# Kernel optimization log

Measured on AMD Instinct MI355X. Metric: run time of the kernel, lower is better.

## Reference

```python
import jax, jax.numpy as jnp
import numpy as np

N = 100000      # num_node
D = 64          # latent_dim
R_EX = 8        # num_relation_ex
R_IM = 4        # num_relation_im
E_EX = 2000000  # explicit edges
E_IM = 1000000  # implicit edges


def setup_inputs() -> dict:
    key = jax.random.key(0)
    ks = jax.random.split(key, 32)
    f = lambda i, shape, s=0.05: jax.random.normal(ks[i], shape, dtype=jnp.float32) * s
    inp = {}
    inp["edge_index_ex"] = jax.random.randint(ks[0], (2, E_EX), 0, N)
    inp["edge_type_ex"] = jax.random.randint(ks[1], (E_EX,), 0, R_EX)
    inp["edge_index_im"] = jax.random.randint(ks[2], (2, E_IM), 0, N)
    inp["edge_type_im"] = jax.random.randint(ks[3], (E_IM,), 0, R_IM)
    # RGCN layer-1 (in_channels = num_node, x=None -> weight acts as per-relation embedding table)
    inp["W1_ex"] = f(4, (R_EX, N, D)); inp["root1_ex"] = f(5, (N, D)); inp["b1_ex"] = f(6, (D,))
    inp["W1_im"] = f(7, (R_IM, N, D)); inp["root1_im"] = f(8, (N, D)); inp["b1_im"] = f(9, (D,))
    # RGCN layer-2 (latent_dim -> latent_dim)
    inp["W2_ex"] = f(10, (R_EX, D, D)); inp["root2_ex"] = f(11, (D, D)); inp["b2_ex"] = f(12, (D,))
    inp["W2_im"] = f(13, (R_IM, D, D)); inp["root2_im"] = f(14, (D, D)); inp["b2_im"] = f(15, (D,))
    # ATTITU fusion head: four Linear(D, 1)
    inp["att_w11"] = f(16, (D,)); inp["att_b11"] = f(17, ())
    inp["att_w12"] = f(18, (D,)); inp["att_b12"] = f(19, ())
    inp["att_w21"] = f(20, (D,)); inp["att_b21"] = f(21, ())
    inp["att_w22"] = f(22, (D,)); inp["att_b22"] = f(23, ())
    # MLP aggregation: Linear(2D, D) -> LeakyReLU -> Linear(D, D)
    inp["agg_W1"] = f(24, (2 * D, D)); inp["agg_b1"] = f(25, (D,))
    inp["agg_W2"] = f(26, (D, D)); inp["agg_b2"] = f(27, (D,))
    return inp


def _rgcn_embed(W, root, bias, src, dst, etype, R):
    # Layer 1, x=None: out_i = root_i + bias + sum_r mean_{e: type(e)=r, dst(e)=i} W[r, src(e)]
    out = root + bias  # [N, D]
    for r in range(R):
        m = (etype == r).astype(jnp.float32)            # [E]
        msg = W[r][src] * m[:, None]                    # [E, D] relation-r embedding gather
        s = jax.ops.segment_sum(msg, dst, num_segments=N)
        c = jax.ops.segment_sum(m, dst, num_segments=N)
        out = out + s / jnp.maximum(c, 1.0)[:, None]
    return out


def _rgcn(x, W, root, bias, src, dst, etype, R):
    # Layer 2: out_i = x_i @ root + bias + sum_r (mean_{e: type=r, dst=i} x[src(e)]) @ W[r]
    out = x @ root + bias
    for r in range(R):
        m = (etype == r).astype(x.dtype)
        msg = x[src] * m[:, None]                        # [E, D]
        s = jax.ops.segment_sum(msg, dst, num_segments=N)
        c = jax.ops.segment_sum(m, dst, num_segments=N)
        h = s / jnp.maximum(c, 1.0)[:, None]             # mean-aggregated, then linear (PyG order)
        out = out + h @ W[r]
    return out


def _attitu(e1, e2, w11, b11, w12, b12, w21, b21, w22, b22):
    s1 = jax.nn.softmax(jnp.stack([e1 @ w11 + b11, e2 @ w12 + b12], axis=1), axis=1)  # [N, 2]
    f1 = s1[:, 0:1] * e1 + s1[:, 1:2] * e2
    s2 = jax.nn.softmax(jnp.stack([e1 @ w21 + b21, e2 @ w22 + b22], axis=1), axis=1)
    f2 = s2[:, 1:2] * e2 + s2[:, 0:1] * e1
    return f1, f2


def reference(edge_index_ex, edge_type_ex, edge_index_im, edge_type_im,
              W1_ex, root1_ex, b1_ex, W1_im, root1_im, b1_im,
              W2_ex, root2_ex, b2_ex, W2_im, root2_im, b2_im,
              att_w11, att_b11, att_w12, att_b12, att_w21, att_b21, att_w22, att_b22,
              agg_W1, agg_b1, agg_W2, agg_b2):
    src_ex, dst_ex = edge_index_ex[0], edge_index_ex[1]
    src_im, dst_im = edge_index_im[0], edge_index_im[1]
    ex_x1 = _rgcn_embed(W1_ex, root1_ex, b1_ex, src_ex, dst_ex, edge_type_ex, R_EX)
    im_x1 = _rgcn_embed(W1_im, root1_im, b1_im, src_im, dst_im, edge_type_im, R_IM)
    t_ex, t_im = _attitu(ex_x1, im_x1, att_w11, att_b11, att_w12, att_b12,
                         att_w21, att_b21, att_w22, att_b22)
    ex_x2 = _rgcn(t_ex, W2_ex, root2_ex, b2_ex, src_ex, dst_ex, edge_type_ex, R_EX)
    im_x2 = _rgcn(t_im, W2_im, root2_im, b2_im, src_im, dst_im, edge_type_im, R_IM)
    cat = jnp.concatenate([ex_x1 + ex_x2, im_x1 + im_x2], axis=1)  # [N, 2D]
    return jax.nn.leaky_relu(cat @ agg_W1 + agg_b1, negative_slope=0.01) @ agg_W2 + agg_b2
```

## Files before the change

### kernel.cpp

```cpp
#include <hip/hip_runtime.h>
#include <hip/hip_bf16.h>

#define N_NODE 100000
#define DIM 64
#define R_EX 8
#define R_IM 4
#define E_EX 2000000
#define E_IM 1000000
#define ND (N_NODE * DIM)

typedef __hip_bfloat16 bf16;

__device__ __forceinline__ float b2f(bf16 v) { return __bfloat162float(v); }

__device__ __forceinline__ float ldv(const void* p, long long i, int f32) {
    return f32 ? ((const float*)p)[i] : b2f(((const bf16*)p)[i]);
}

__global__ void detect_kernel(const void* probe, int* flag) {
    int t = threadIdx.x;
    float v = b2f(((const bf16*)probe)[t]);
    int bad = !(fabsf(v) <= 4.0f);
    unsigned long long m = __ballot(bad);
    if (t == 0) *flag = (m != 0ull) ? 1 : 0;
}

__global__ void count_kernel(const int* __restrict__ eidx, const int* __restrict__ etype,
                             float* __restrict__ cnt, int E) {
    int e = blockIdx.x * blockDim.x + threadIdx.x;
    if (e >= E) return;
    int dst = eidx[E + e];
    int r = etype[e];
    atomicAdd(&cnt[r * N_NODE + dst], 1.0f);
}

__global__ void inv_kernel(float* __restrict__ cnt, int n) {
    int i = blockIdx.x * blockDim.x + threadIdx.x;
    if (i >= n) return;
    cnt[i] = 1.0f / fmaxf(cnt[i], 1.0f);
}

__global__ void l1_init(const void* __restrict__ root, const void* __restrict__ bias,
                        const int* __restrict__ fp, float* __restrict__ x1) {
    int i = blockIdx.x * blockDim.x + threadIdx.x;
    if (i >= ND) return;
    int f32 = *fp;
    x1[i] = ldv(root, i, f32) + ldv(bias, i & (DIM - 1), f32);
}

__global__ void l1_edge(const int* __restrict__ eidx, const int* __restrict__ etype,
                        const void* __restrict__ W1, const float* __restrict__ inv,
                        const int* __restrict__ fp, float* __restrict__ x1, int E) {
    int gid = blockIdx.x * blockDim.x + threadIdx.x;
    int e = gid >> 6;
    int d = gid & 63;
    if (e >= E) return;
    int f32 = *fp;
    int src = eidx[e];
    int dst = eidx[E + e];
    int r = etype[e];
    float w = inv[r * N_NODE + dst];
    float v = ldv(W1, ((long long)r * N_NODE + src) * DIM + d, f32);
    atomicAdd(&x1[dst * DIM + d], v * w);
}

__global__ void attitu_kernel(const float* __restrict__ ex1, const float* __restrict__ im1,
                              const void* __restrict__ w11, const void* __restrict__ b11,
                              const void* __restrict__ w12, const void* __restrict__ b12,
                              const void* __restrict__ w21, const void* __restrict__ b21,
                              const void* __restrict__ w22, const void* __restrict__ b22,
                              const int* __restrict__ fp,
                              float* __restrict__ t_ex, float* __restrict__ t_im) {
    int gid = blockIdx.x * blockDim.x + threadIdx.x;
    int i = gid >> 6;
    int d = gid & 63;
    if (i >= N_NODE) return;
    int f32 = *fp;
    float e1 = ex1[i * DIM + d];
    float e2 = im1[i * DIM + d];
    float p11 = e1 * ldv(w11, d, f32);
    float p12 = e2 * ldv(w12, d, f32);
    float p21 = e1 * ldv(w21, d, f32);
    float p22 = e2 * ldv(w22, d, f32);
#pragma unroll
    for (int off = 32; off; off >>= 1) {
        p11 += __shfl_xor(p11, off);
        p12 += __shfl_xor(p12, off);
        p21 += __shfl_xor(p21, off);
        p22 += __shfl_xor(p22, off);
    }
    float a11 = p11 + ldv(b11, 0, f32);
    float a12 = p12 + ldv(b12, 0, f32);
    float a21 = p21 + ldv(b21, 0, f32);
    float a22 = p22 + ldv(b22, 0, f32);

    float m1 = fmaxf(a11, a12);
    float z11 = __expf(a11 - m1), z12 = __expf(a12 - m1);
    float i1 = 1.0f / (z11 + z12);
    float s10 = z11 * i1, s11 = z12 * i1;

    float m2 = fmaxf(a21, a22);
    float z21 = __expf(a21 - m2), z22 = __expf(a22 - m2);
    float i2 = 1.0f / (z21 + z22);
    float s20 = z21 * i2, s21 = z22 * i2;

    t_ex[i * DIM + d] = s10 * e1 + s11 * e2;
    t_im[i * DIM + d] = s20 * e1 + s21 * e2;
}

__global__ void l2_init_fused(const float* __restrict__ t, const void* __restrict__ root2,
                              const void* __restrict__ b2, const int* __restrict__ fp,
                              float* __restrict__ x1) {
    int gid = blockIdx.x * blockDim.x + threadIdx.x;
    int i = gid >> 6;
    int d = gid & 63;
    if (i >= N_NODE) return;
    int f32 = *fp;
    float tv = t[i * DIM + d];
    float acc = ldv(b2, d, f32) + x1[i * DIM + d];
    if (f32) {
        const float* W = (const float*)root2;
#pragma unroll
        for (int k = 0; k < DIM; ++k) acc += __shfl(tv, k) * W[k * DIM + d];
    } else {
        const bf16* W = (const bf16*)root2;
#pragma unroll
        for (int k = 0; k < DIM; ++k) acc += __shfl(tv, k) * b2f(W[k * DIM + d]);
    }
    x1[i * DIM + d] = acc;
}

__global__ void l2_agg(const int* __restrict__ eidx, const int* __restrict__ etype,
                       const float* __restrict__ t, float* __restrict__ h,
                       int E, int r0, int rc) {
    int gid = blockIdx.x * blockDim.x + threadIdx.x;
    int e = gid >> 6;
    int d = gid & 63;
    if (e >= E) return;
    int r = etype[e] - r0;
    if ((unsigned)r >= (unsigned)rc) return;
    int src = eidx[e];
    int dst = eidx[E + e];
    atomicAdd(&h[(long long)r * ND + dst * DIM + d], t[src * DIM + d]);
}

__global__ void l2_dense(const float* __restrict__ h, const void* __restrict__ W2,
                         const float* __restrict__ inv, const int* __restrict__ fp,
                         float* __restrict__ a2, int r0, int rc) {
    int gid = blockIdx.x * blockDim.x + threadIdx.x;
    int i = gid >> 6;
    int d = gid & 63;
    if (i >= N_NODE) return;
    int f32 = *fp;
    float acc = a2[i * DIM + d];
    for (int c = 0; c < rc; ++c) {
        float hv = h[(long long)c * ND + i * DIM + d];
        float w = inv[(r0 + c) * N_NODE + i];
        float s = 0.0f;
        if (f32) {
            const float* W = (const float*)W2 + (r0 + c) * DIM * DIM;
#pragma unroll
            for (int k = 0; k < DIM; ++k) s += __shfl(hv, k) * W[k * DIM + d];
        } else {
            const bf16* W = (const bf16*)W2 + (r0 + c) * DIM * DIM;
#pragma unroll
            for (int k = 0; k < DIM; ++k) s += __shfl(hv, k) * b2f(W[k * DIM + d]);
        }
        acc += w * s;
    }
    a2[i * DIM + d] = acc;
}

__global__ void l2_edge(const int* __restrict__ eidx, const int* __restrict__ etype,
                        const float* __restrict__ t, const void* __restrict__ W2,
                        const float* __restrict__ inv, const int* __restrict__ fp,
                        float* __restrict__ a2, int E) {
    int gid = blockIdx.x * blockDim.x + threadIdx.x;
    int e = gid >> 6;
    int d = gid & 63;
    if (e >= E) return;
    int f32 = *fp;
    int src = eidx[e];
    int dst = eidx[E + e];
    int r = etype[e];
    float tv = t[src * DIM + d];
    float acc = 0.0f;
    if (f32) {
        const float* W = (const float*)W2 + r * DIM * DIM;
#pragma unroll
        for (int k = 0; k < DIM; ++k) acc += __shfl(tv, k) * W[k * DIM + d];
    } else {
        const bf16* W = (const bf16*)W2 + r * DIM * DIM;
#pragma unroll
        for (int k = 0; k < DIM; ++k) acc += __shfl(tv, k) * b2f(W[k * DIM + d]);
    }
    float w = inv[r * N_NODE + dst];
    atomicAdd(&a2[dst * DIM + d], acc * w);
}

__global__ void final_kernel(const float* __restrict__ a2ex, const float* __restrict__ a2im,
                             const void* __restrict__ aggW1, const void* __restrict__ aggb1,
                             const void* __restrict__ aggW2, const void* __restrict__ aggb2,
                             const int* __restrict__ fp, void* __restrict__ out) {
    int gid = blockIdx.x * blockDim.x + threadIdx.x;
    int i = gid >> 6;
    int d = gid & 63;
    if (i >= N_NODE) return;
    int f32 = *fp;
    float cex = a2ex[i * DIM + d];
    float cim = a2im[i * DIM + d];
    float h = ldv(aggb1, d, f32);
    if (f32) {
        const float* W = (const float*)aggW1;
#pragma unroll
        for (int k = 0; k < DIM; ++k) {
            h += __shfl(cex, k) * W[k * DIM + d];
            h += __shfl(cim, k) * W[(DIM + k) * DIM + d];
        }
    } else {
        const bf16* W = (const bf16*)aggW1;
#pragma unroll
        for (int k = 0; k < DIM; ++k) {
            h += __shfl(cex, k) * b2f(W[k * DIM + d]);
            h += __shfl(cim, k) * b2f(W[(DIM + k) * DIM + d]);
        }
    }
    h = (h > 0.0f) ? h : 0.01f * h;
    float o = ldv(aggb2, d, f32);
    if (f32) {
        const float* W = (const float*)aggW2;
#pragma unroll
        for (int k = 0; k < DIM; ++k) o += __shfl(h, k) * W[k * DIM + d];
        ((float*)out)[i * DIM + d] = o;
    } else {
        const bf16* W = (const bf16*)aggW2;
#pragma unroll
        for (int k = 0; k < DIM; ++k) o += __shfl(h, k) * b2f(W[k * DIM + d]);
        ((bf16*)out)[i * DIM + d] = __float2bfloat16(o);
    }
}

extern "C" void kernel_launch(void* const* d_in, const int* in_sizes, int n_in,
                              void* d_out, int out_size, void* d_ws, size_t ws_size,
                              hipStream_t stream) {
    const int* eidx_ex  = (const int*)d_in[0];
    const int* etype_ex = (const int*)d_in[1];
    const int* eidx_im  = (const int*)d_in[2];
    const int* etype_im = (const int*)d_in[3];
    const void* W1_ex   = d_in[4];
    const void* root1_ex= d_in[5];
    const void* b1_ex   = d_in[6];
    const void* W1_im   = d_in[7];
    const void* root1_im= d_in[8];
    const void* b1_im   = d_in[9];
    const void* W2_ex   = d_in[10];
    const void* root2_ex= d_in[11];
    const void* b2_ex   = d_in[12];
    const void* W2_im   = d_in[13];
    const void* root2_im= d_in[14];
    const void* b2_im   = d_in[15];
    const void* att_w11 = d_in[16];
    const void* att_b11 = d_in[17];
    const void* att_w12 = d_in[18];
    const void* att_b12 = d_in[19];
    const void* att_w21 = d_in[20];
    const void* att_b21 = d_in[21];
    const void* att_w22 = d_in[22];
    const void* att_b22 = d_in[23];
    const void* agg_W1  = d_in[24];
    const void* agg_b1  = d_in[25];
    const void* agg_W2  = d_in[26];
    const void* agg_b2  = d_in[27];

    float* ws = (float*)d_ws;
    int*   flag   = (int*)d_ws;
    float* inv_ex = ws + 64;
    float* inv_im = inv_ex + R_EX * N_NODE;
    float* x1ex   = inv_im + R_IM * N_NODE;
    float* x1im   = x1ex + ND;
    float* t_ex   = x1im + ND;
    float* t_im   = t_ex + ND;
    float* hbuf   = t_im + ND;

    const long long base_floats = 64 + (long long)(R_EX + R_IM) * N_NODE + 4LL * ND;
    long long avail = (long long)(ws_size / sizeof(float)) - base_floats;
    int cmax = (avail > 0) ? (int)(avail / ND) : 0;
    if (cmax > R_EX) cmax = R_EX;

    const int B = 256;

    detect_kernel<<<1, 64, 0, stream>>>(b1_ex, flag);

    hipMemsetAsync(inv_ex, 0, (size_t)(R_EX + R_IM) * N_NODE * sizeof(float), stream);
    count_kernel<<<(E_EX + B - 1) / B, B, 0, stream>>>(eidx_ex, etype_ex, inv_ex, E_EX);
    count_kernel<<<(E_IM + B - 1) / B, B, 0, stream>>>(eidx_im, etype_im, inv_im, E_IM);
    inv_kernel<<<((R_EX + R_IM) * N_NODE + B - 1) / B, B, 0, stream>>>(inv_ex, (R_EX + R_IM) * N_NODE);

    l1_init<<<(ND + B - 1) / B, B, 0, stream>>>(root1_ex, b1_ex, flag, x1ex);
    l1_init<<<(ND + B - 1) / B, B, 0, stream>>>(root1_im, b1_im, flag, x1im);
    l1_edge<<<(E_EX * 64) / B, B, 0, stream>>>(eidx_ex, etype_ex, W1_ex, inv_ex, flag, x1ex, E_EX);
    l1_edge<<<(E_IM * 64) / B, B, 0, stream>>>(eidx_im, etype_im, W1_im, inv_im, flag, x1im, E_IM);

    attitu_kernel<<<(N_NODE * 64 + B - 1) / B, B, 0, stream>>>(
        x1ex, x1im, att_w11, att_b11, att_w12, att_b12, att_w21, att_b21, att_w22, att_b22,
        flag, t_ex, t_im);

    l2_init_fused<<<(N_NODE * 64 + B - 1) / B, B, 0, stream>>>(t_ex, root2_ex, b2_ex, flag, x1ex);
    l2_init_fused<<<(N_NODE * 64 + B - 1) / B, B, 0, stream>>>(t_im, root2_im, b2_im, flag, x1im);

    if (cmax >= 1) {
        for (int r0 = 0; r0 < R_EX; r0 += cmax) {
            int rc = (R_EX - r0 < cmax) ? (R_EX - r0) : cmax;
            hipMemsetAsync(hbuf, 0, (size_t)rc * ND * sizeof(float), stream);
            l2_agg<<<(E_EX * 64) / B, B, 0, stream>>>(eidx_ex, etype_ex, t_ex, hbuf, E_EX, r0, rc);
            l2_dense<<<(N_NODE * 64 + B - 1) / B, B, 0, stream>>>(hbuf, W2_ex, inv_ex, flag, x1ex, r0, rc);
        }
        for (int r0 = 0; r0 < R_IM; r0 += cmax) {
            int rc = (R_IM - r0 < cmax) ? (R_IM - r0) : cmax;
            hipMemsetAsync(hbuf, 0, (size_t)rc * ND * sizeof(float), stream);
            l2_agg<<<(E_IM * 64) / B, B, 0, stream>>>(eidx_im, etype_im, t_im, hbuf, E_IM, r0, rc);
            l2_dense<<<(N_NODE * 64 + B - 1) / B, B, 0, stream>>>(hbuf, W2_im, inv_im, flag, x1im, r0, rc);
        }
    } else {
        l2_edge<<<(E_EX * 64) / B, B, 0, stream>>>(eidx_ex, etype_ex, t_ex, W2_ex, inv_ex, flag, x1ex, E_EX);
        l2_edge<<<(E_IM * 64) / B, B, 0, stream>>>(eidx_im, etype_im, t_im, W2_im, inv_im, flag, x1im, E_IM);
    }

    final_kernel<<<(N_NODE * 64 + B - 1) / B, B, 0, stream>>>(
        x1ex, x1im, agg_W1, agg_b1, agg_W2, agg_b2, flag, (void*)d_out);
}
```

Measured before the change: 3.233 ms.

## Keep weight columns in registers and loop nodes per wave in dense kernels

The dense per-node matvec kernels (l2_init, l2_dense, final) now run on a fixed grid. Each wave keeps its weight column in registers and loops over a contiguous range of nodes, reading rows with broadcast float4 loads instead of using 64 shuffles plus weight loads per node. The inverse-degree scaling moves from the dense kernel into the scatter-add, and the final MLP is split into two kernels with a temporary buffer. The change trades the repeated weight reloads and shuffles for higher register use, a serial per-wave loop, and an extra write and read of the hidden activations.

```diff
diff --git a/kernel.cpp b/kernel.cpp
--- a/kernel.cpp
+++ b/kernel.cpp
@@ -8,6 +8,7 @@
 #define E_EX 2000000
 #define E_IM 1000000
 #define ND (N_NODE * DIM)
+#define NGRID 1024
 
 typedef __hip_bfloat16 bf16;
 
@@ -111,64 +112,95 @@
 __global__ void l2_init_fused(const float* __restrict__ t, const void* __restrict__ root2,
                               const void* __restrict__ b2, const int* __restrict__ fp,
                               float* __restrict__ x1) {
-    int gid = blockIdx.x * blockDim.x + threadIdx.x;
-    int i = gid >> 6;
-    int d = gid & 63;
-    if (i >= N_NODE) return;
-    int f32 = *fp;
-    float tv = t[i * DIM + d];
-    float acc = ldv(b2, d, f32) + x1[i * DIM + d];
+    int wid = (blockIdx.x * blockDim.x + threadIdx.x) >> 6;
+    int d = threadIdx.x & 63;
+    int nwaves = (gridDim.x * blockDim.x) >> 6;
+    int per = (N_NODE + nwaves - 1) / nwaves;
+    int i0 = wid * per;
+    int i1 = (i0 + per < N_NODE) ? i0 + per : N_NODE;
+    if (i0 >= i1) return;
+    int f32 = *fp;
+    float Wreg[DIM];
     if (f32) {
         const float* W = (const float*)root2;
 #pragma unroll
-        for (int k = 0; k < DIM; ++k) acc += __shfl(tv, k) * W[k * DIM + d];
+        for (int k = 0; k < DIM; ++k) Wreg[k] = W[k * DIM + d];
     } else {
         const bf16* W = (const bf16*)root2;
 #pragma unroll
-        for (int k = 0; k < DIM; ++k) acc += __shfl(tv, k) * b2f(W[k * DIM + d]);
-    }
-    x1[i * DIM + d] = acc;
+        for (int k = 0; k < DIM; ++k) Wreg[k] = b2f(W[k * DIM + d]);
+    }
+    float bv = ldv(b2, d, f32);
+    for (int i = i0; i < i1; ++i) {
+        const float4* row = (const float4*)(t + (long long)i * DIM);
+        float acc0 = 0.0f, acc1 = 0.0f;
+#pragma unroll
+        for (int q = 0; q < DIM / 8; ++q) {
+            float4 u = row[2 * q];
+            float4 v = row[2 * q + 1];
+            acc0 += u.x * Wreg[8 * q + 0]; acc0 += u.y * Wreg[8 * q + 1];
+            acc0 += u.z * Wreg[8 * q + 2]; acc0 += u.w * Wreg[8 * q + 3];
+            acc1 += v.x * Wreg[8 * q + 4]; acc1 += v.y * Wreg[8 * q + 5];
+            acc1 += v.z * Wreg[8 * q + 6]; acc1 += v.w * Wreg[8 * q + 7];
+        }
+        x1[(long long)i * DIM + d] += bv + acc0 + acc1;
+    }
 }
 
 __global__ void l2_agg(const int* __restrict__ eidx, const int* __restrict__ etype,
-                       const float* __restrict__ t, float* __restrict__ h,
-                       int E, int r0, int rc) {
+                       const float* __restrict__ t, const float* __restrict__ inv,
+                       float* __restrict__ h, int E, int r0, int rc) {
     int gid = blockIdx.x * blockDim.x + threadIdx.x;
     int e = gid >> 6;
     int d = gid & 63;
     if (e >= E) return;
-    int r = etype[e] - r0;
-    if ((unsigned)r >= (unsigned)rc) return;
+    int r = etype[e];
+    int rl = r - r0;
+    if ((unsigned)rl >= (unsigned)rc) return;
     int src = eidx[e];
     int dst = eidx[E + e];
-    atomicAdd(&h[(long long)r * ND + dst * DIM + d], t[src * DIM + d]);
+    float w = inv[r * N_NODE + dst];
+    atomicAdd(&h[(long long)rl * ND + dst * DIM + d], t[src * DIM + d] * w);
 }
 
 __global__ void l2_dense(const float* __restrict__ h, const void* __restrict__ W2,
-                         const float* __restrict__ inv, const int* __restrict__ fp,
-                         float* __restrict__ a2, int r0, int rc) {
-    int gid = blockIdx.x * blockDim.x + threadIdx.x;
-    int i = gid >> 6;
-    int d = gid & 63;
-    if (i >= N_NODE) return;
-    int f32 = *fp;
-    float acc = a2[i * DIM + d];
+                         const int* __restrict__ fp, float* __restrict__ a2,
+                         int r0, int rc) {
+    int wid = (blockIdx.x * blockDim.x + threadIdx.x) >> 6;
+    int d = threadIdx.x & 63;
+    int nwaves = (gridDim.x * blockDim.x) >> 6;
+    int per = (N_NODE + nwaves - 1) / nwaves;
+    int i0 = wid * per;
+    int i1 = (i0 + per < N_NODE) ? i0 + per : N_NODE;
+    if (i0 >= i1) return;
+    int f32 = *fp;
     for (int c = 0; c < rc; ++c) {
-        float hv = h[(long long)c * ND + i * DIM + d];
-        float w = inv[(r0 + c) * N_NODE + i];
-        float s = 0.0f;
+        float Wreg[DIM];
         if (f32) {
-            const float* W = (const float*)W2 + (r0 + c) * DIM * DIM;
-#pragma unroll
-            for (int k = 0; k < DIM; ++k) s += __shfl(hv, k) * W[k * DIM + d];
+            const float* W = (const float*)W2 + (long long)(r0 + c) * DIM * DIM;
+#pragma unroll
+            for (int k = 0; k < DIM; ++k) Wreg[k] = W[k * DIM + d];
         } else {
-            const bf16* W = (const bf16*)W2 + (r0 + c) * DIM * DIM;
-#pragma unroll
-            for (int k = 0; k < DIM; ++k) s += __shfl(hv, k) * b2f(W[k * DIM + d]);
-        }
-        acc += w * s;
-    }
-    a2[i * DIM + d] = acc;
+            const bf16* W = (const bf16*)W2 + (long long)(r0 + c) * DIM * DIM;
+#pragma unroll
+            for (int k = 0; k < DIM; ++k) Wreg[k] = b2f(W[k * DIM + d]);
+        }
+        const float* hc = h + (long long)c * ND;
+        for (int i = i0; i < i1; ++i) {
+            const float4* row = (const float4*)(hc + (long long)i * DIM);
+            float acc0 = 0.0f, acc1 = 0.0f;
+#pragma unroll
+            for (int q = 0; q < DIM / 8; ++q) {
+                float4 u = row[2 * q];
+                float4 v = row[2 * q + 1];
+                acc0 += u.x * Wreg[8 * q + 0]; acc0 += u.y * Wreg[8 * q + 1];
+                acc0 += u.z * Wreg[8 * q + 2]; acc0 += u.w * Wreg[8 * q + 3];
+                acc1 += v.x * Wreg[8 * q + 4]; acc1 += v.y * Wreg[8 * q + 5];
+                acc1 += v.z * Wreg[8 * q + 6]; acc1 += v.w * Wreg[8 * q + 7];
+            }
+            a2[(long long)i * DIM + d] += acc0 + acc1;
+        }
+    }
 }
 
 __global__ void l2_edge(const int* __restrict__ eidx, const int* __restrict__ etype,
@@ -198,45 +230,92 @@
     atomicAdd(&a2[dst * DIM + d], acc * w);
 }
 
-__global__ void final_kernel(const float* __restrict__ a2ex, const float* __restrict__ a2im,
-                             const void* __restrict__ aggW1, const void* __restrict__ aggb1,
-                             const void* __restrict__ aggW2, const void* __restrict__ aggb2,
-                             const int* __restrict__ fp, void* __restrict__ out) {
-    int gid = blockIdx.x * blockDim.x + threadIdx.x;
-    int i = gid >> 6;
-    int d = gid & 63;
-    if (i >= N_NODE) return;
-    int f32 = *fp;
-    float cex = a2ex[i * DIM + d];
-    float cim = a2im[i * DIM + d];
-    float h = ldv(aggb1, d, f32);
+__global__ void final_a(const float* __restrict__ a2ex, const float* __restrict__ a2im,
+                        const void* __restrict__ aggW1, const void* __restrict__ aggb1,
+                        const int* __restrict__ fp, float* __restrict__ tmp) {
+    int wid = (blockIdx.x * blockDim.x + threadIdx.x) >> 6;
+    int d = threadIdx.x & 63;
+    int nwaves = (gridDim.x * blockDim.x) >> 6;
+    int per = (N_NODE + nwaves - 1) / nwaves;
+    int i0 = wid * per;
+    int i1 = (i0 + per < N_NODE) ? i0 + per : N_NODE;
+    if (i0 >= i1) return;
+    int f32 = *fp;
+    float Wa[DIM], Wb[DIM];
     if (f32) {
         const float* W = (const float*)aggW1;
 #pragma unroll
-        for (int k = 0; k < DIM; ++k) {
-            h += __shfl(cex, k) * W[k * DIM + d];
-            h += __shfl(cim, k) * W[(DIM + k) * DIM + d];
-        }
+        for (int k = 0; k < DIM; ++k) { Wa[k] = W[k * DIM + d]; Wb[k] = W[(DIM + k) * DIM + d]; }
     } else {
         const bf16* W = (const bf16*)aggW1;
 #pragma unroll
-        for (int k = 0; k < DIM; ++k) {
-            h += __shfl(cex, k) * b2f(W[k * DIM + d]);
-            h += __shfl(cim, k) * b2f(W[(DIM + k) * DIM + d]);
-        }
-    }
-    h = (h > 0.0f) ? h : 0.01f * h;
-    float o = ldv(aggb2, d, f32);
+        for (int k = 0; k < DIM; ++k) { Wa[k] = b2f(W[k * DIM + d]); Wb[k] = b2f(W[(DIM + k) * DIM + d]); }
+    }
+    float bv = ldv(aggb1, d, f32);
+    for (int i = i0; i < i1; ++i) {
+        const float4* ra = (const float4*)(a2ex + (long long)i * DIM);
+        const float4* rb = (const float4*)(a2im + (long long)i * DIM);
+        float acc0 = bv, acc1 = 0.0f;
+#pragma unroll
+        for (int q = 0; q < DIM / 8; ++q) {
+            float4 u = ra[2 * q];
+            float4 v = ra[2 * q + 1];
+            acc0 += u.x * Wa[8 * q + 0]; acc0 += u.y * Wa[8 * q + 1];
+            acc0 += u.z * Wa[8 * q + 2]; acc0 += u.w * Wa[8 * q + 3];
+            acc1 += v.x * Wa[8 * q + 4]; acc1 += v.y * Wa[8 * q + 5];
+            acc1 += v.z * Wa[8 * q + 6]; acc1 += v.w * Wa[8 * q + 7];
+        }
+#pragma unroll
+        for (int q = 0; q < DIM / 8; ++q) {
+            float4 u = rb[2 * q];
+            float4 v = rb[2 * q + 1];
+            acc0 += u.x * Wb[8 * q + 0]; acc0 += u.y * Wb[8 * q + 1];
+            acc0 += u.z * Wb[8 * q + 2]; acc0 += u.w * Wb[8 * q + 3];
+            acc1 += v.x * Wb[8 * q + 4]; acc1 += v.y * Wb[8 * q + 5];
+            acc1 += v.z * Wb[8 * q + 6]; acc1 += v.w * Wb[8 * q + 7];
+        }
+        float hv = acc0 + acc1;
+        tmp[(long long)i * DIM + d] = (hv > 0.0f) ? hv : 0.01f * hv;
+    }
+}
+
+__global__ void final_b(const float* __restrict__ tmp, const void* __restrict__ aggW2,
+                        const void* __restrict__ aggb2, const int* __restrict__ fp,
+                        void* __restrict__ out) {
+    int wid = (blockIdx.x * blockDim.x + threadIdx.x) >> 6;
+    int d = threadIdx.x & 63;
+    int nwaves = (gridDim.x * blockDim.x) >> 6;
+    int per = (N_NODE + nwaves - 1) / nwaves;
+    int i0 = wid * per;
+    int i1 = (i0 + per < N_NODE) ? i0 + per : N_NODE;
+    if (i0 >= i1) return;
+    int f32 = *fp;
+    float Wreg[DIM];
     if (f32) {
         const float* W = (const float*)aggW2;
 #pragma unroll
-        for (int k = 0; k < DIM; ++k) o += __shfl(h, k) * W[k * DIM + d];
-        ((float*)out)[i * DIM + d] = o;
+        for (int k = 0; k < DIM; ++k) Wreg[k] = W[k * DIM + d];
     } else {
         const bf16* W = (const bf16*)aggW2;
 #pragma unroll
-        for (int k = 0; k < DIM; ++k) o += __shfl(h, k) * b2f(W[k * DIM + d]);
-        ((bf16*)out)[i * DIM + d] = __float2bfloat16(o);
+        for (int k = 0; k < DIM; ++k) Wreg[k] = b2f(W[k * DIM + d]);
+    }
+    float bv = ldv(aggb2, d, f32);
+    for (int i = i0; i < i1; ++i) {
+        const float4* row = (const float4*)(tmp + (long long)i * DIM);
+        float acc0 = bv, acc1 = 0.0f;
+#pragma unroll
+        for (int q = 0; q < DIM / 8; ++q) {
+            float4 u = row[2 * q];
+            float4 v = row[2 * q + 1];
+            acc0 += u.x * Wreg[8 * q + 0]; acc0 += u.y * Wreg[8 * q + 1];
+            acc0 += u.z * Wreg[8 * q + 2]; acc0 += u.w * Wreg[8 * q + 3];
+            acc1 += v.x * Wreg[8 * q + 4]; acc1 += v.y * Wreg[8 * q + 5];
+            acc1 += v.z * Wreg[8 * q + 6]; acc1 += v.w * Wreg[8 * q + 7];
+        }
+        float o = acc0 + acc1;
+        if (f32) ((float*)out)[(long long)i * DIM + d] = o;
+        else ((bf16*)out)[(long long)i * DIM + d] = __float2bfloat16(o);
     }
 }
 
@@ -305,27 +384,27 @@
         x1ex, x1im, att_w11, att_b11, att_w12, att_b12, att_w21, att_b21, att_w22, att_b22,
         flag, t_ex, t_im);
 
-    l2_init_fused<<<(N_NODE * 64 + B - 1) / B, B, 0, stream>>>(t_ex, root2_ex, b2_ex, flag, x1ex);
-    l2_init_fused<<<(N_NODE * 64 + B - 1) / B, B, 0, stream>>>(t_im, root2_im, b2_im, flag, x1im);
+    l2_init_fused<<<NGRID, B, 0, stream>>>(t_ex, root2_ex, b2_ex, flag, x1ex);
+    l2_init_fused<<<NGRID, B, 0, stream>>>(t_im, root2_im, b2_im, flag, x1im);
 
     if (cmax >= 1) {
         for (int r0 = 0; r0 < R_EX; r0 += cmax) {
             int rc = (R_EX - r0 < cmax) ? (R_EX - r0) : cmax;
             hipMemsetAsync(hbuf, 0, (size_t)rc * ND * sizeof(float), stream);
-            l2_agg<<<(E_EX * 64) / B, B, 0, stream>>>(eidx_ex, etype_ex, t_ex, hbuf, E_EX, r0, rc);
-            l2_dense<<<(N_NODE * 64 + B - 1) / B, B, 0, stream>>>(hbuf, W2_ex, inv_ex, flag, x1ex, r0, rc);
+            l2_agg<<<(E_EX * 64) / B, B, 0, stream>>>(eidx_ex, etype_ex, t_ex, inv_ex, hbuf, E_EX, r0, rc);
+            l2_dense<<<NGRID, B, 0, stream>>>(hbuf, W2_ex, flag, x1ex, r0, rc);
         }
         for (int r0 = 0; r0 < R_IM; r0 += cmax) {
             int rc = (R_IM - r0 < cmax) ? (R_IM - r0) : cmax;
             hipMemsetAsync(hbuf, 0, (size_t)rc * ND * sizeof(float), stream);
-            l2_agg<<<(E_IM * 64) / B, B, 0, stream>>>(eidx_im, etype_im, t_im, hbuf, E_IM, r0, rc);
-            l2_dense<<<(N_NODE * 64 + B - 1) / B, B, 0, stream>>>(hbuf, W2_im, inv_im, flag, x1im, r0, rc);
+            l2_agg<<<(E_IM * 64) / B, B, 0, stream>>>(eidx_im, etype_im, t_im, inv_im, hbuf, E_IM, r0, rc);
+            l2_dense<<<NGRID, B, 0, stream>>>(hbuf, W2_im, flag, x1im, r0, rc);
         }
     } else {
         l2_edge<<<(E_EX * 64) / B, B, 0, stream>>>(eidx_ex, etype_ex, t_ex, W2_ex, inv_ex, flag, x1ex, E_EX);
         l2_edge<<<(E_IM * 64) / B, B, 0, stream>>>(eidx_im, etype_im, t_im, W2_im, inv_im, flag, x1im, E_IM);
     }
 
-    final_kernel<<<(N_NODE * 64 + B - 1) / B, B, 0, stream>>>(
-        x1ex, x1im, agg_W1, agg_b1, agg_W2, agg_b2, flag, (void*)d_out);
-}
+    final_a<<<NGRID, B, 0, stream>>>(x1ex, x1im, agg_W1, agg_b1, flag, t_ex);
+    final_b<<<NGRID, B, 0, stream>>>(t_ex, agg_W2, agg_b2, flag, d_out);
+}
```

Result: slower. 5.376 ms (+66.3%).
